# Optimization experiments

Hardware: AMD Instinct MI355X
Metric: run time of the kernel (lower is better)

## Reference

```python
import jax, jax.numpy as jnp
import numpy as np

B, S, D = 4, 1024, 1280
H, DH = 20, 64          # n_head, d_hidden = embed_dim // n_head
DF = 4 * D              # r_ff = 4


def setup_inputs() -> dict:
    key = jax.random.key(0)
    ks = jax.random.split(key, 8)
    s_qkv = 1.0 / np.sqrt(D)
    inp = {
        "x": jax.random.normal(ks[0], (B, S, D), dtype=jnp.float32),
        # projection weights stored [in, out] so y = x @ W
        "Wq": jax.random.normal(ks[1], (D, H * DH), dtype=jnp.float32) * s_qkv,
        "Wk": jax.random.normal(ks[2], (D, H * DH), dtype=jnp.float32) * s_qkv,
        "Wv": jax.random.normal(ks[3], (D, H * DH), dtype=jnp.float32) * s_qkv,
        "ln_g": jnp.ones((D,), dtype=jnp.float32),
        "ln_b": jnp.zeros((D,), dtype=jnp.float32),
        "W1": jax.random.normal(ks[4], (D, DF), dtype=jnp.float32) * np.sqrt(2.0 / D),
        "b1": jnp.zeros((DF,), dtype=jnp.float32),
        "W2": jax.random.normal(ks[5], (DF, D), dtype=jnp.float32) * (1.0 / np.sqrt(DF)),
        "b2": jnp.zeros((D,), dtype=jnp.float32),
    }
    return inp


def reference(x, Wq, Wk, Wv, ln_g, ln_b, W1, b1, W2, b2):
    scaling = 1.0 / np.sqrt(DH)
    # --- Attention (note: original forward never applies to_out) ---
    q = (x @ Wq).reshape(B, S, H, DH) * scaling
    k = (x @ Wk).reshape(B, S, H, DH)
    v = (x @ Wv).reshape(B, S, H, DH)
    attn = jnp.einsum('bqhd,bkhd->bhqk', q, k)
    attn = jax.nn.softmax(attn, axis=-1)
    out = jnp.einsum('bhqk,bkhd->bqhd', attn, v).reshape(B, S, H * DH)
    x = out + x  # residual
    # --- FeedForward: LayerNorm -> linear1 -> relu -> linear2, residual ---
    mu = jnp.mean(x, axis=-1, keepdims=True)
    var = jnp.mean(jnp.square(x - mu), axis=-1, keepdims=True)
    h = (x - mu) * jax.lax.rsqrt(var + 1e-5) * ln_g + ln_b
    h = jax.nn.relu(h @ W1 + b1)
    h = h @ W2 + b2
    return x + h
```

## Files before the change

kernel.cpp:

```cpp
#include <hip/hip_runtime.h>
#include <hip/hip_bf16.h>

typedef short bf16x8 __attribute__((ext_vector_type(8)));
typedef float f32x4 __attribute__((ext_vector_type(4)));

typedef unsigned int u32_as1 __attribute__((address_space(1)));
typedef unsigned int u32_as3 __attribute__((address_space(3)));

#define B_ 4
#define S_ 1024
#define D_ 1280
#define H_ 20
#define DH_ 64
#define DF_ 5120
#define BS_ (B_*S_)
#define NQKV 3840

__device__ __forceinline__ void gld_lds16(const __hip_bfloat16* g, __hip_bfloat16* l) {
  __builtin_amdgcn_global_load_lds((const u32_as1*)g, (u32_as3*)l, 16, 0, 0);
}

__global__ __launch_bounds__(256) void cvt_f2b(
    const float* __restrict__ in, __hip_bfloat16* __restrict__ out, int n4)
{
  int i = blockIdx.x * 256 + threadIdx.x;
  if (i >= n4) return;
  const float4 v = ((const float4*)in)[i];
  __hip_bfloat16 o[4] = {__float2bfloat16(v.x), __float2bfloat16(v.y),
                         __float2bfloat16(v.z), __float2bfloat16(v.w)};
  *(short4*)(out + (size_t)i * 4) = *(short4*)o;
}

__global__ __launch_bounds__(256) void transpose_f2b(
    const float* __restrict__ in, __hip_bfloat16* __restrict__ out,
    int K, int N)
{
  __shared__ float tile[32][33];
  int k0 = blockIdx.x * 32, n0 = blockIdx.y * 32;
  int tx = threadIdx.x & 31, ty = threadIdx.x >> 5;
  #pragma unroll
  for (int i = 0; i < 32; i += 8)
    tile[ty + i][tx] = in[(size_t)(k0 + ty + i) * N + n0 + tx];
  __syncthreads();
  #pragma unroll
  for (int i = 0; i < 32; i += 8)
    out[(size_t)(n0 + ty + i) * K + k0 + tx] = __float2bfloat16(tile[tx][ty + i]);
}

__global__ __launch_bounds__(256) void transpose_v(
    const __hip_bfloat16* __restrict__ qkv, __hip_bfloat16* __restrict__ vT)
{
  __shared__ __hip_bfloat16 tile[32][33];
  int s0 = blockIdx.x * 32;
  int d0 = blockIdx.y * 32;
  int bh = blockIdx.z;
  int b = bh / H_, h = bh - b * H_;
  int tx = threadIdx.x & 31, ty = threadIdx.x >> 5;
  const __hip_bfloat16* src = qkv + (size_t)b * S_ * NQKV + 2 * D_ + h * DH_;
  #pragma unroll
  for (int i = 0; i < 32; i += 8)
    tile[ty + i][tx] = src[(size_t)(s0 + ty + i) * NQKV + d0 + tx];
  __syncthreads();
  __hip_bfloat16* dst = vT + (size_t)bh * DH_ * S_;
  #pragma unroll
  for (int i = 0; i < 32; i += 8)
    dst[(size_t)(d0 + ty + i) * S_ + s0 + tx] = tile[tx][ty + i];
}

template<int EPI>
__global__ __launch_bounds__(256, 1) void gemm256(
    const __hip_bfloat16* __restrict__ A,
    const __hip_bfloat16* __restrict__ BT,
    const float* __restrict__ bias,
    __hip_bfloat16* __restrict__ C,
    float* __restrict__ Cf0,
    float* __restrict__ Cf1,
    float* __restrict__ Cf2,
    int M, int N, int K, int KextA, int KextR)
{
  __shared__ __align__(16) __hip_bfloat16 As[2][2][256 * 32];
  __shared__ __align__(16) __hip_bfloat16 Bs[2][2][256 * 32];
  __hip_bfloat16* AsF = &As[0][0][0];
  __hip_bfloat16* BsF = &Bs[0][0][0];

  const int t = threadIdx.x;
  const int lane = t & 63;
  const int wave = t >> 6;
  const int wm = wave >> 1, wn = wave & 1;
  const int quad = lane >> 4, l16 = lane & 15;

  const int gx = gridDim.x;
  const int nwg = gx * gridDim.y;
  int orig = blockIdx.y * gx + blockIdx.x;
  int bx = blockIdx.x, by = blockIdx.y;
  if ((nwg & 7) == 0) {
    const int q = nwg >> 3;
    const int swz = (orig & 7) * q + (orig >> 3);
    bx = swz % gx; by = swz / gx;
  }
  const int bm = bx * 256, bn = by * 256;

  const int z = blockIdx.z;
  const int koff = (z == 0) ? 0 : (KextA + (z - 1) * KextR);
  const int Kc = (z == 0) ? KextA : KextR;
  const int NT = Kc >> 6;

  const int sc = (t & 3) ^ ((t >> 3) & 3);
  const __hip_bfloat16* Ag = A  + (size_t)(bm + (t >> 2)) * K + koff + sc * 8;
  const __hip_bfloat16* Bg = BT + (size_t)(bn + (t >> 2)) * K + koff + sc * 8;
  const size_t rq = (size_t)64 * K;

  const int swzf = quad ^ ((l16 >> 1) & 3);
  const int aob = (wm * 128 + l16) * 32 + swzf * 8;
  const int bob = (wn * 128 + l16) * 32 + swzf * 8;

  f32x4 acc[8][8];
  #pragma unroll
  for (int i = 0; i < 8; i++)
    #pragma unroll
    for (int j = 0; j < 8; j++)
      acc[i][j] = (f32x4){0.f, 0.f, 0.f, 0.f};

#define STAGE(u_, bb_) do { \
    const size_t co_ = (size_t)(u_) * 64; \
    _Pragma("unroll") \
    for (int q = 0; q < 4; q++) { \
      gld_lds16(Ag + co_ + q * rq,      AsF + ((bb_) * 2 + 0) * 8192 + q * 2048 + t * 8); \
      gld_lds16(Ag + co_ + 32 + q * rq, AsF + ((bb_) * 2 + 1) * 8192 + q * 2048 + t * 8); \
      gld_lds16(Bg + co_ + q * rq,      BsF + ((bb_) * 2 + 0) * 8192 + q * 2048 + t * 8); \
      gld_lds16(Bg + co_ + 32 + q * rq, BsF + ((bb_) * 2 + 1) * 8192 + q * 2048 + t * 8); \
    } \
  } while (0)

  STAGE(0, 0);
  asm volatile("s_waitcnt vmcnt(0)" ::: "memory");
  __builtin_amdgcn_s_barrier();
  asm volatile("" ::: "memory");

  for (int u = 0; u < NT; ++u) {
    const int bb = u & 1;
    const int hb0 = (bb * 2 + 0) * 8192, hb1 = (bb * 2 + 1) * 8192;

    bf16x8 av[8], bv[8], aw[8], bw[8];
    #pragma unroll
    for (int mi = 0; mi < 8; mi++) av[mi] = *(const bf16x8*)(AsF + hb0 + aob + mi * 512);
    #pragma unroll
    for (int nj = 0; nj < 8; nj++) bv[nj] = *(const bf16x8*)(BsF + hb0 + bob + nj * 512);
    if (u + 1 < NT) STAGE(u + 1, bb ^ 1);
    #pragma unroll
    for (int mi = 0; mi < 8; mi++) aw[mi] = *(const bf16x8*)(AsF + hb1 + aob + mi * 512);
    #pragma unroll
    for (int nj = 0; nj < 8; nj++) bw[nj] = *(const bf16x8*)(BsF + hb1 + bob + nj * 512);

    #pragma unroll
    for (int mi = 0; mi < 8; mi++)
      #pragma unroll
      for (int nj = 0; nj < 8; nj++)
        acc[mi][nj] = __builtin_amdgcn_mfma_f32_16x16x32_bf16(av[mi], bv[nj], acc[mi][nj], 0, 0, 0);
    #pragma unroll
    for (int mi = 0; mi < 8; mi++)
      #pragma unroll
      for (int nj = 0; nj < 8; nj++)
        acc[mi][nj] = __builtin_amdgcn_mfma_f32_16x16x32_bf16(aw[mi], bw[nj], acc[mi][nj], 0, 0, 0);

    if (u + 1 < NT) { asm volatile("s_waitcnt vmcnt(0)" ::: "memory"); }
    asm volatile("" ::: "memory");
    __builtin_amdgcn_s_barrier();
    asm volatile("" ::: "memory");
  }

#undef STAGE

  float* Cf = (z == 0) ? Cf0 : ((z == 1) ? Cf1 : Cf2);
  #pragma unroll
  for (int i = 0; i < 8; i++) {
    #pragma unroll
    for (int j = 0; j < 8; j++) {
      int col = bn + wn * 128 + j * 16 + l16;
      #pragma unroll
      for (int r = 0; r < 4; r++) {
        int row = bm + wm * 128 + i * 16 + quad * 4 + r;
        float v = acc[i][j][r];
        if (EPI == 1) { v += bias[col]; v = fmaxf(v, 0.f); }
        if (EPI == 3) {
          Cf[(size_t)row * N + col] = v;
        } else {
          C[(size_t)row * N + col] = __float2bfloat16(v);
        }
      }
    }
  }
}

__global__ __launch_bounds__(256) void ffn2_reduce3(
    const float* __restrict__ P0, const float* __restrict__ P1,
    const float* __restrict__ bias, const float* __restrict__ resid,
    float* __restrict__ out)
{
  int i = blockIdx.x * 256 + threadIdx.x;
  float4 p0 = ((const float4*)P0)[i];
  float4 p1 = ((const float4*)P1)[i];
  float4 p2 = ((const float4*)out)[i];
  float4 r  = ((const float4*)resid)[i];
  float4 b  = ((const float4*)bias)[i % (D_ / 4)];
  float4 o;
  o.x = p0.x + p1.x + p2.x + r.x + b.x;
  o.y = p0.y + p1.y + p2.y + r.y + b.y;
  o.z = p0.z + p1.z + p2.z + r.z + b.z;
  o.w = p0.w + p1.w + p2.w + r.w + b.w;
  ((float4*)out)[i] = o;
}

__global__ __launch_bounds__(256) void attn_mfma(
    const __hip_bfloat16* __restrict__ qkv,
    const __hip_bfloat16* __restrict__ vT,
    const float* __restrict__ x,
    float* __restrict__ x1)
{
  const int qt = blockIdx.x, h = blockIdx.y, b = blockIdx.z;
  const int t = threadIdx.x;
  const int lane = t & 63;
  const int wave = t >> 6;
  const int quad = lane >> 4, l16 = lane & 15;

  __shared__ __hip_bfloat16 Ks[2][64 * 64];
  __shared__ __hip_bfloat16 Vs[2][64 * 64];
  __shared__ short Pl[4][16][72];

  const int qrow0 = qt * 128 + wave * 32;
  const size_t tok0 = (size_t)b * S_;
  const int qcol = h * DH_;
  const int kcol = D_ + h * DH_;
  const size_t vtbase = (size_t)(b * H_ + h) * DH_ * S_;

  const int s1i = t + 256;
  const int r0 = t >> 3,   c0 = (t & 7)   ^ (r0 & 7);
  const int r1 = s1i >> 3, c1 = (s1i & 7) ^ (r1 & 7);
  const __hip_bfloat16* Kg0 = qkv + (tok0 + r0) * NQKV + kcol + c0 * 8;
  const __hip_bfloat16* Kg1 = qkv + (tok0 + r1) * NQKV + kcol + c1 * 8;
  const __hip_bfloat16* Vg0 = vT + vtbase + (size_t)r0 * S_ + c0 * 8;
  const __hip_bfloat16* Vg1 = vT + vtbase + (size_t)r1 * S_ + c1 * 8;
  const size_t kstep = (size_t)64 * NQKV;

  const float qscale = 0.125f * 1.44269504088896340736f;
  bf16x8 aq[2][2];
  #pragma unroll
  for (int m = 0; m < 2; m++)
    #pragma unroll
    for (int kc = 0; kc < 2; kc++) {
      bf16x8 raw = *(const bf16x8*)(qkv + (tok0 + qrow0 + m * 16 + l16) * NQKV
                                        + qcol + kc * 32 + quad * 8);
      bf16x8 scaled;
      #pragma unroll
      for (int j = 0; j < 8; j++) {
        float f = __uint_as_float(((unsigned)(unsigned short)raw[j]) << 16) * qscale;
        __hip_bfloat16 hb = __float2bfloat16(f);
        scaled[j] = *reinterpret_cast<short*>(&hb);
      }
      aq[m][kc] = scaled;
    }

  f32x4 O[2][4];
  float lsum[2][4];
  #pragma unroll
  for (int m = 0; m < 2; m++)
    #pragma unroll
    for (int n = 0; n < 4; n++) O[m][n] = (f32x4){0.f, 0.f, 0.f, 0.f};
  #pragma unroll
  for (int m = 0; m < 2; m++)
    #pragma unroll
    for (int r = 0; r < 4; r++) lsum[m][r] = 0.f;

  gld_lds16(Kg0, &Ks[0][t * 8]);
  gld_lds16(Kg1, &Ks[0][t * 8 + 2048]);
  gld_lds16(Vg0, &Vs[0][t * 8]);
  gld_lds16(Vg1, &Vs[0][t * 8 + 2048]);

  const int fsw = l16 & 7;

  for (int kt = 0; kt < S_ / 64; kt++) {
    const int buf = kt & 1;
    __syncthreads();

    if (kt + 1 < S_ / 64) {
      const int nb = buf ^ 1;
      gld_lds16(Kg0 + (size_t)(kt + 1) * kstep, &Ks[nb][t * 8]);
      gld_lds16(Kg1 + (size_t)(kt + 1) * kstep, &Ks[nb][t * 8 + 2048]);
      gld_lds16(Vg0 + (kt + 1) * 64, &Vs[nb][t * 8]);
      gld_lds16(Vg1 + (kt + 1) * 64, &Vs[nb][t * 8 + 2048]);
    }

    bf16x8 kb[4][2];
    #pragma unroll
    for (int j = 0; j < 4; j++)
      #pragma unroll
      for (int kc = 0; kc < 2; kc++)
        kb[j][kc] = *(const bf16x8*)&Ks[buf][(j * 16 + l16) * 64
                                            + (((kc * 4 + quad) ^ fsw) * 8)];
    f32x4 sc[2][4];
    #pragma unroll
    for (int m = 0; m < 2; m++)
      #pragma unroll
      for (int j = 0; j < 4; j++) {
        sc[m][j] = (f32x4){0.f, 0.f, 0.f, 0.f};
        sc[m][j] = __builtin_amdgcn_mfma_f32_16x16x32_bf16(aq[m][0], kb[j][0], sc[m][j], 0, 0, 0);
        sc[m][j] = __builtin_amdgcn_mfma_f32_16x16x32_bf16(aq[m][1], kb[j][1], sc[m][j], 0, 0, 0);
      }

    bf16x8 vb[4][2];
    #pragma unroll
    for (int n = 0; n < 4; n++)
      #pragma unroll
      for (int kc = 0; kc < 2; kc++)
        vb[n][kc] = *(const bf16x8*)&Vs[buf][(n * 16 + l16) * 64
                                            + (((kc * 4 + quad) ^ fsw) * 8)];

    #pragma unroll
    for (int m = 0; m < 2; m++) {
      #pragma unroll
      for (int j = 0; j < 4; j++)
        #pragma unroll
        for (int r = 0; r < 4; r++) {
          float p = exp2f(sc[m][j][r]);
          lsum[m][r] += p;
          Pl[wave][quad * 4 + r][j * 16 + l16] = (short)(__float_as_uint(p) >> 16);
        }
      bf16x8 pa0 = *(const bf16x8*)&Pl[wave][l16][quad * 8];
      bf16x8 pa1 = *(const bf16x8*)&Pl[wave][l16][32 + quad * 8];
      #pragma unroll
      for (int n = 0; n < 4; n++) {
        O[m][n] = __builtin_amdgcn_mfma_f32_16x16x32_bf16(pa0, vb[n][0], O[m][n], 0, 0, 0);
        O[m][n] = __builtin_amdgcn_mfma_f32_16x16x32_bf16(pa1, vb[n][1], O[m][n], 0, 0, 0);
      }
    }
  }

  #pragma unroll
  for (int m = 0; m < 2; m++)
    #pragma unroll
    for (int r = 0; r < 4; r++) {
      float s = lsum[m][r];
      s += __shfl_xor(s, 1);
      s += __shfl_xor(s, 2);
      s += __shfl_xor(s, 4);
      s += __shfl_xor(s, 8);
      lsum[m][r] = 1.f / s;
    }

  #pragma unroll
  for (int m = 0; m < 2; m++)
    #pragma unroll
    for (int n = 0; n < 4; n++)
      #pragma unroll
      for (int r = 0; r < 4; r++) {
        size_t row = tok0 + qrow0 + m * 16 + quad * 4 + r;
        int col = qcol + n * 16 + l16;
        size_t idx = row * D_ + col;
        x1[idx] = O[m][n][r] * lsum[m][r] + x[idx];
      }
}

__global__ __launch_bounds__(256) void ln_kernel(
    const float* __restrict__ x1, const float* __restrict__ g,
    const float* __restrict__ bta, __hip_bfloat16* __restrict__ h)
{
  int row = blockIdx.x, t = threadIdx.x;
  __shared__ float red[256];
  float v[5];
  size_t base = (size_t)row * D_;
  #pragma unroll
  for (int i = 0; i < 5; i++) v[i] = x1[base + t + 256 * i];
  float s = v[0] + v[1] + v[2] + v[3] + v[4];
  red[t] = s; __syncthreads();
  for (int off = 128; off; off >>= 1) {
    if (t < off) red[t] += red[t + off];
    __syncthreads();
  }
  float mu = red[0] * (1.f / D_);
  __syncthreads();
  float sq = 0.f;
  #pragma unroll
  for (int i = 0; i < 5; i++) { float d = v[i] - mu; sq += d * d; }
  red[t] = sq; __syncthreads();
  for (int off = 128; off; off >>= 1) {
    if (t < off) red[t] += red[t + off];
    __syncthreads();
  }
  float rs = rsqrtf(red[0] * (1.f / D_) + 1e-5f);
  #pragma unroll
  for (int i = 0; i < 5; i++) {
    int c = t + 256 * i;
    float hv = (v[i] - mu) * rs * g[c] + bta[c];
    h[base + c] = __float2bfloat16(hv);
  }
}

extern "C" void kernel_launch(void* const* d_in, const int* in_sizes, int n_in,
                              void* d_out, int out_size, void* d_ws, size_t ws_size,
                              hipStream_t stream) {
  (void)in_sizes; (void)n_in; (void)out_size; (void)ws_size;
  const float* x   = (const float*)d_in[0];
  const float* Wq  = (const float*)d_in[1];
  const float* Wk  = (const float*)d_in[2];
  const float* Wv  = (const float*)d_in[3];
  const float* lng = (const float*)d_in[4];
  const float* lnb = (const float*)d_in[5];
  const float* W1  = (const float*)d_in[6];
  const float* b1  = (const float*)d_in[7];
  const float* W2  = (const float*)d_in[8];
  const float* b2  = (const float*)d_in[9];
  float* out = (float*)d_out;

  char* ws = (char*)d_ws;
  size_t o = 0;
  __hip_bfloat16* W2T = (__hip_bfloat16*)(ws + o); o += (size_t)D_ * DF_ * 2;
  float*          x1  = (float*)(ws + o);          o += (size_t)BS_ * D_ * 4;
  char* regA = ws + o; o += (size_t)DF_ * D_ * 2 + (size_t)BS_ * D_ * 2;
  __hip_bfloat16* W1T  = (__hip_bfloat16*)regA;
  __hip_bfloat16* hbuf = (__hip_bfloat16*)(regA + (size_t)DF_ * D_ * 2);
  float*          P0   = (float*)regA;
  char* regB = ws + o;
  __hip_bfloat16* xb    = (__hip_bfloat16*)regB;
  __hip_bfloat16* BTqkv = (__hip_bfloat16*)(regB + (size_t)BS_ * D_ * 2);
  __hip_bfloat16* qkv   = (__hip_bfloat16*)(regB + (size_t)BS_ * D_ * 2
                                                 + (size_t)NQKV * D_ * 2);
  __hip_bfloat16* vT    = (__hip_bfloat16*)(regB + (size_t)BS_ * D_ * 2
                                                 + (size_t)NQKV * D_ * 2
                                                 + (size_t)BS_ * NQKV * 2);
  float*          P1    = (float*)regB;
  __hip_bfloat16* gbuf  = (__hip_bfloat16*)(regB + (size_t)BS_ * D_ * 4);
  float*          P2    = out;

  transpose_f2b<<<dim3(D_/32, D_/32), 256, 0, stream>>>(Wq, BTqkv,                   D_, D_);
  transpose_f2b<<<dim3(D_/32, D_/32), 256, 0, stream>>>(Wk, BTqkv + (size_t)D_*D_,   D_, D_);
  transpose_f2b<<<dim3(D_/32, D_/32), 256, 0, stream>>>(Wv, BTqkv + (size_t)2*D_*D_, D_, D_);
  transpose_f2b<<<dim3(D_/32, DF_/32), 256, 0, stream>>>(W1, W1T, D_, DF_);
  transpose_f2b<<<dim3(DF_/32, D_/32), 256, 0, stream>>>(W2, W2T, DF_, D_);
  cvt_f2b<<<(BS_*D_/4 + 255)/256, 256, 0, stream>>>(x, xb, BS_*D_/4);

  gemm256<0><<<dim3(BS_/256, NQKV/256), 256, 0, stream>>>(
      xb, BTqkv, nullptr, qkv, nullptr, nullptr, nullptr, BS_, NQKV, D_, D_, D_);
  transpose_v<<<dim3(S_/32, DH_/32, B_*H_), 256, 0, stream>>>(qkv, vT);
  attn_mfma<<<dim3(S_/128, H_, B_), 256, 0, stream>>>(qkv, vT, x, x1);
  ln_kernel<<<BS_, 256, 0, stream>>>(x1, lng, lnb, hbuf);
  gemm256<1><<<dim3(BS_/256, DF_/256), 256, 0, stream>>>(
      hbuf, W1T, b1, gbuf, nullptr, nullptr, nullptr, BS_, DF_, D_, D_, D_);
  gemm256<3><<<dim3(BS_/256, D_/256, 3), 256, 0, stream>>>(
      gbuf, W2T, nullptr, nullptr, P0, P1, P2, BS_, D_, DF_, 1792, 1664);
  ffn2_reduce3<<<BS_*D_/4/256, 256, 0, stream>>>(P0, P1, b2, x1, out);
}
```

Baseline: 443.3 us.

## Retile GEMM to 8 waves of 128x64 with two blocks per CU

The bf16 GEMM kernel goes from 256 threads (4 waves, each owning a 128x128 sub-tile) to 512 threads (8 waves, each owning 128x64), with launch bounds of (512, 2). This cuts per-wave accumulator registers so more waves can hide LDS and MFMA latency. The LDS fragment loads are split into smaller chunks interleaved with MFMA groups, and the next-stage global-to-LDS prefetch is now issued before any compute. The grouped block-index swizzle is removed, so blocks map directly to tiles, which may reduce L2 reuse across neighbouring workgroups.

```diff
diff --git a/kernel.cpp b/kernel.cpp
--- a/kernel.cpp
+++ b/kernel.cpp
@@ -68,7 +68,7 @@
 }
 
 template<int EPI>
-__global__ __launch_bounds__(256, 1) void gemm256(
+__global__ __launch_bounds__(512, 2) void gemm256(
     const __hip_bfloat16* __restrict__ A,
     const __hip_bfloat16* __restrict__ BT,
     const float* __restrict__ bias,
@@ -86,53 +86,48 @@
   const int t = threadIdx.x;
   const int lane = t & 63;
   const int wave = t >> 6;
-  const int wm = wave >> 1, wn = wave & 1;
+  const int wm = wave >> 2, wn = wave & 3;
   const int quad = lane >> 4, l16 = lane & 15;
-
-  const int gx = gridDim.x;
-  const int nwg = gx * gridDim.y;
-  int orig = blockIdx.y * gx + blockIdx.x;
-  int bx = blockIdx.x, by = blockIdx.y;
-  if ((nwg & 7) == 0) {
-    const int q = nwg >> 3;
-    const int swz = (orig & 7) * q + (orig >> 3);
-    bx = swz % gx; by = swz / gx;
-  }
-  const int bm = bx * 256, bn = by * 256;
+  const int bm = blockIdx.x * 256, bn = blockIdx.y * 256;
 
   const int z = blockIdx.z;
   const int koff = (z == 0) ? 0 : (KextA + (z - 1) * KextR);
   const int Kc = (z == 0) ? KextA : KextR;
   const int NT = Kc >> 6;
 
+  const int srow = t >> 2;
   const int sc = (t & 3) ^ ((t >> 3) & 3);
-  const __hip_bfloat16* Ag = A  + (size_t)(bm + (t >> 2)) * K + koff + sc * 8;
-  const __hip_bfloat16* Bg = BT + (size_t)(bn + (t >> 2)) * K + koff + sc * 8;
-  const size_t rq = (size_t)64 * K;
+  const __hip_bfloat16* Ag = A  + (size_t)(bm + srow) * K + koff + sc * 8;
+  const __hip_bfloat16* Bg = BT + (size_t)(bn + srow) * K + koff + sc * 8;
+  const size_t rq = (size_t)128 * K;
 
   const int swzf = quad ^ ((l16 >> 1) & 3);
   const int aob = (wm * 128 + l16) * 32 + swzf * 8;
-  const int bob = (wn * 128 + l16) * 32 + swzf * 8;
-
-  f32x4 acc[8][8];
+  const int bob = (wn * 64 + l16) * 32 + swzf * 8;
+
+  f32x4 acc[8][4];
   #pragma unroll
   for (int i = 0; i < 8; i++)
     #pragma unroll
-    for (int j = 0; j < 8; j++)
+    for (int j = 0; j < 4; j++)
       acc[i][j] = (f32x4){0.f, 0.f, 0.f, 0.f};
 
-#define STAGE(u_, bb_) do { \
-    const size_t co_ = (size_t)(u_) * 64; \
-    _Pragma("unroll") \
-    for (int q = 0; q < 4; q++) { \
-      gld_lds16(Ag + co_ + q * rq,      AsF + ((bb_) * 2 + 0) * 8192 + q * 2048 + t * 8); \
-      gld_lds16(Ag + co_ + 32 + q * rq, AsF + ((bb_) * 2 + 1) * 8192 + q * 2048 + t * 8); \
-      gld_lds16(Bg + co_ + q * rq,      BsF + ((bb_) * 2 + 0) * 8192 + q * 2048 + t * 8); \
-      gld_lds16(Bg + co_ + 32 + q * rq, BsF + ((bb_) * 2 + 1) * 8192 + q * 2048 + t * 8); \
-    } \
+#define STAGE_A(u_, kk_, b_) do { \
+    const __hip_bfloat16* g_ = Ag + (size_t)(u_) * 64 + (kk_) * 32; \
+    gld_lds16(g_,      AsF + ((b_) * 2 + (kk_)) * 8192 + t * 8); \
+    gld_lds16(g_ + rq, AsF + ((b_) * 2 + (kk_)) * 8192 + 4096 + t * 8); \
   } while (0)
-
-  STAGE(0, 0);
+#define STAGE_B(u_, kk_, b_) do { \
+    const __hip_bfloat16* g_ = Bg + (size_t)(u_) * 64 + (kk_) * 32; \
+    gld_lds16(g_,      BsF + ((b_) * 2 + (kk_)) * 8192 + t * 8); \
+    gld_lds16(g_ + rq, BsF + ((b_) * 2 + (kk_)) * 8192 + 4096 + t * 8); \
+  } while (0)
+#define STAGE_ALL(u_, b_) do { \
+    STAGE_A(u_, 0, b_); STAGE_B(u_, 0, b_); \
+    STAGE_A(u_, 1, b_); STAGE_B(u_, 1, b_); \
+  } while (0)
+
+  STAGE_ALL(0, 0);
   asm volatile("s_waitcnt vmcnt(0)" ::: "memory");
   __builtin_amdgcn_s_barrier();
   asm volatile("" ::: "memory");
@@ -141,42 +136,57 @@
     const int bb = u & 1;
     const int hb0 = (bb * 2 + 0) * 8192, hb1 = (bb * 2 + 1) * 8192;
 
-    bf16x8 av[8], bv[8], aw[8], bw[8];
-    #pragma unroll
-    for (int mi = 0; mi < 8; mi++) av[mi] = *(const bf16x8*)(AsF + hb0 + aob + mi * 512);
-    #pragma unroll
-    for (int nj = 0; nj < 8; nj++) bv[nj] = *(const bf16x8*)(BsF + hb0 + bob + nj * 512);
-    if (u + 1 < NT) STAGE(u + 1, bb ^ 1);
-    #pragma unroll
-    for (int mi = 0; mi < 8; mi++) aw[mi] = *(const bf16x8*)(AsF + hb1 + aob + mi * 512);
-    #pragma unroll
-    for (int nj = 0; nj < 8; nj++) bw[nj] = *(const bf16x8*)(BsF + hb1 + bob + nj * 512);
-
-    #pragma unroll
-    for (int mi = 0; mi < 8; mi++)
-      #pragma unroll
-      for (int nj = 0; nj < 8; nj++)
-        acc[mi][nj] = __builtin_amdgcn_mfma_f32_16x16x32_bf16(av[mi], bv[nj], acc[mi][nj], 0, 0, 0);
-    #pragma unroll
-    for (int mi = 0; mi < 8; mi++)
-      #pragma unroll
-      for (int nj = 0; nj < 8; nj++)
-        acc[mi][nj] = __builtin_amdgcn_mfma_f32_16x16x32_bf16(aw[mi], bw[nj], acc[mi][nj], 0, 0, 0);
+    if (u + 1 < NT) STAGE_ALL(u + 1, bb ^ 1);
+
+    bf16x8 av[4], bv[4];
+    #pragma unroll
+    for (int i = 0; i < 4; i++) av[i] = *(const bf16x8*)(AsF + hb0 + aob + i * 512);
+    #pragma unroll
+    for (int j = 0; j < 4; j++) bv[j] = *(const bf16x8*)(BsF + hb0 + bob + j * 512);
+    #pragma unroll
+    for (int i = 0; i < 4; i++)
+      #pragma unroll
+      for (int j = 0; j < 4; j++)
+        acc[i][j] = __builtin_amdgcn_mfma_f32_16x16x32_bf16(av[i], bv[j], acc[i][j], 0, 0, 0);
+    #pragma unroll
+    for (int i = 0; i < 4; i++) av[i] = *(const bf16x8*)(AsF + hb0 + aob + (i + 4) * 512);
+    #pragma unroll
+    for (int i = 0; i < 4; i++)
+      #pragma unroll
+      for (int j = 0; j < 4; j++)
+        acc[i + 4][j] = __builtin_amdgcn_mfma_f32_16x16x32_bf16(av[i], bv[j], acc[i + 4][j], 0, 0, 0);
+    #pragma unroll
+    for (int i = 0; i < 4; i++) av[i] = *(const bf16x8*)(AsF + hb1 + aob + i * 512);
+    #pragma unroll
+    for (int j = 0; j < 4; j++) bv[j] = *(const bf16x8*)(BsF + hb1 + bob + j * 512);
+    #pragma unroll
+    for (int i = 0; i < 4; i++)
+      #pragma unroll
+      for (int j = 0; j < 4; j++)
+        acc[i][j] = __builtin_amdgcn_mfma_f32_16x16x32_bf16(av[i], bv[j], acc[i][j], 0, 0, 0);
+    #pragma unroll
+    for (int i = 0; i < 4; i++) av[i] = *(const bf16x8*)(AsF + hb1 + aob + (i + 4) * 512);
+    #pragma unroll
+    for (int i = 0; i < 4; i++)
+      #pragma unroll
+      for (int j = 0; j < 4; j++)
+        acc[i + 4][j] = __builtin_amdgcn_mfma_f32_16x16x32_bf16(av[i], bv[j], acc[i + 4][j], 0, 0, 0);
 
     if (u + 1 < NT) { asm volatile("s_waitcnt vmcnt(0)" ::: "memory"); }
-    asm volatile("" ::: "memory");
     __builtin_amdgcn_s_barrier();
     asm volatile("" ::: "memory");
   }
 
-#undef STAGE
+#undef STAGE_ALL
+#undef STAGE_B
+#undef STAGE_A
 
   float* Cf = (z == 0) ? Cf0 : ((z == 1) ? Cf1 : Cf2);
   #pragma unroll
   for (int i = 0; i < 8; i++) {
     #pragma unroll
-    for (int j = 0; j < 8; j++) {
-      int col = bn + wn * 128 + j * 16 + l16;
+    for (int j = 0; j < 4; j++) {
+      int col = bn + wn * 64 + j * 16 + l16;
       #pragma unroll
       for (int r = 0; r < 4; r++) {
         int row = bm + wm * 128 + i * 16 + quad * 4 + r;
@@ -438,14 +448,14 @@
   transpose_f2b<<<dim3(DF_/32, D_/32), 256, 0, stream>>>(W2, W2T, DF_, D_);
   cvt_f2b<<<(BS_*D_/4 + 255)/256, 256, 0, stream>>>(x, xb, BS_*D_/4);
 
-  gemm256<0><<<dim3(BS_/256, NQKV/256), 256, 0, stream>>>(
+  gemm256<0><<<dim3(BS_/256, NQKV/256), 512, 0, stream>>>(
       xb, BTqkv, nullptr, qkv, nullptr, nullptr, nullptr, BS_, NQKV, D_, D_, D_);
   transpose_v<<<dim3(S_/32, DH_/32, B_*H_), 256, 0, stream>>>(qkv, vT);
   attn_mfma<<<dim3(S_/128, H_, B_), 256, 0, stream>>>(qkv, vT, x, x1);
   ln_kernel<<<BS_, 256, 0, stream>>>(x1, lng, lnb, hbuf);
-  gemm256<1><<<dim3(BS_/256, DF_/256), 256, 0, stream>>>(
+  gemm256<1><<<dim3(BS_/256, DF_/256), 512, 0, stream>>>(
       hbuf, W1T, b1, gbuf, nullptr, nullptr, nullptr, BS_, DF_, D_, D_, D_);
-  gemm256<3><<<dim3(BS_/256, D_/256, 3), 256, 0, stream>>>(
+  gemm256<3><<<dim3(BS_/256, D_/256, 3), 512, 0, stream>>>(
       gbuf, W2T, nullptr, nullptr, P0, P1, P2, BS_, D_, DF_, 1792, 1664);
   ffn2_reduce3<<<BS_*D_/4/256, 256, 0, stream>>>(P0, P1, b2, x1, out);
 }
```

Result: slower. 458.3 us (+3.4%).
